# Kernel optimization log

Hardware: AMD Instinct MI355X
Metric: run time of the kernel (lower is better)

The kernel has to match this reference:

```python
import jax, jax.numpy as jnp
import numpy as np
import math

LMAX = 3  # max output/input angular momentum degree


def _cg(j1, m1, j2, m2, j, m):
    """Clebsch-Gordan coefficient <j1 m1 j2 m2 | j m> (Condon-Shortley)."""
    if m1 + m2 != m or not (abs(j1 - j2) <= j <= j1 + j2):
        return 0.0
    f = math.factorial
    pref = math.sqrt(
        (2 * j + 1)
        * f(j + j1 - j2) * f(j - j1 + j2) * f(j1 + j2 - j) / f(j1 + j2 + j + 1)
        * f(j + m) * f(j - m) * f(j1 - m1) * f(j1 + m1) * f(j2 - m2) * f(j2 + m2)
    )
    kmin = max(0, j2 - j - m1, j1 - j + m2)
    kmax = min(j1 + j2 - j, j1 - m1, j2 + m2)
    s = 0.0
    for k in range(kmin, kmax + 1):
        s += (-1) ** k / (
            f(k) * f(j1 + j2 - j - k) * f(j1 - m1 - k) * f(j2 + m2 - k)
            * f(j - j2 + m1 + k) * f(j - j1 - m2 + k)
        )
    return pref * s


def _cg_mat(l1, l2, l):
    C = np.zeros((2 * l1 + 1, 2 * l2 + 1, 2 * l + 1), dtype=np.float32)
    for m1 in range(-l1, l1 + 1):
        for m2 in range(-l2, l2 + 1):
            m = m1 + m2
            if abs(m) <= l:
                C[m1 + l1, m2 + l2, m + l] = _cg(l1, m1, l2, m2, l, m)
    return C


_CG = {}
for _l1 in range(LMAX + 1):
    for _l2 in range(LMAX + 1):
        for _l in range(abs(_l1 - _l2), min(_l1 + _l2, LMAX) + 1):
            _CG[(_l1, _l2, _l)] = jnp.asarray(_cg_mat(_l1, _l2, _l))


def _cg_product(A, B):
    """Full CG tensor product of two SO3 vec-arrays.

    A[l], B[l]: (2=complex, N, 2l+1, tau). Output degree l collects, for every
    (l1, l2) pair with |l1-l2| <= l <= l1+l2, the channel outer product
    contracted against the CG matrix (cormorant CGProduct semantics).
    """
    parts = [[] for _ in range(LMAX + 1)]
    for l1 in range(LMAX + 1):
        for l2 in range(LMAX + 1):
            Ar, Ai = A[l1][0], A[l1][1]  # (N, 2l1+1, tau1)
            Br, Bi = B[l2][0], B[l2][1]  # (N, 2l2+1, tau2)
            for l in range(abs(l1 - l2), min(l1 + l2, LMAX) + 1):
                C = _CG[(l1, l2, l)]  # (2l1+1, 2l2+1, 2l+1)
                Tr = (jnp.einsum('xyz,nxc,nyd->nzcd', C, Ar, Br)
                      - jnp.einsum('xyz,nxc,nyd->nzcd', C, Ai, Bi))
                Ti = (jnp.einsum('xyz,nxc,nyd->nzcd', C, Ar, Bi)
                      + jnp.einsum('xyz,nxc,nyd->nzcd', C, Ai, Br))
                n = Tr.shape[0]
                T = jnp.stack([Tr, Ti], axis=0).reshape(2, n, 2 * l + 1, -1)
                parts[l].append(T)
    return tuple(jnp.concatenate(p, axis=-1) for p in parts)


def setup_inputs() -> dict:
    key = jax.random.key(0)
    keys = jax.random.split(key, 8)
    N, TAU = 1024, 16
    d = {}
    for l in range(LMAX + 1):
        d[f'A{l}'] = jax.random.normal(keys[l], (2, N, 2 * l + 1, TAU), dtype=jnp.float32)
        d[f'B{l}'] = jax.random.normal(keys[4 + l], (2, N, 2 * l + 1, TAU), dtype=jnp.float32)
    return d


def reference(A0, A1, A2, A3, B0, B1, B2, B3):
    return _cg_product([A0, A1, A2, A3], [B0, B1, B2, B3])
```

## Files before the change

kernel.cpp:

```cpp
#include <hip/hip_runtime.h>


__device__ inline double dfact(int n) {
    double r = 1.0;
    for (int i = 2; i <= n; ++i) r *= (double)i;
    return r;
}

__device__ double cg_coef(int j1, int m1, int j2, int m2, int j, int m) {
    if (m1 + m2 != m) return 0.0;
    double pref = sqrt((double)(2 * j + 1)
        * dfact(j + j1 - j2) * dfact(j - j1 + j2) * dfact(j1 + j2 - j)
        / dfact(j1 + j2 + j + 1)
        * dfact(j + m) * dfact(j - m) * dfact(j1 - m1) * dfact(j1 + m1)
        * dfact(j2 - m2) * dfact(j2 + m2));
    int kmin = 0;
    if (j2 - j - m1 > kmin) kmin = j2 - j - m1;
    if (j1 - j + m2 > kmin) kmin = j1 - j + m2;
    int kmax = j1 + j2 - j;
    if (j1 - m1 < kmax) kmax = j1 - m1;
    if (j2 + m2 < kmax) kmax = j2 + m2;
    double s = 0.0;
    for (int k = kmin; k <= kmax; ++k) {
        double d = dfact(k) * dfact(j1 + j2 - j - k) * dfact(j1 - m1 - k)
                 * dfact(j2 + m2 - k) * dfact(j - j2 + m1 + k)
                 * dfact(j - j1 - m2 + k);
        s += (k & 1) ? (-1.0 / d) : (1.0 / d);
    }
    return pref * s;
}

__global__ void cg_init_kernel(float* __restrict__ cgbuf) {
    int tid = blockIdx.x * blockDim.x + threadIdx.x;
    int off = 0;
    for (int l1 = 0; l1 <= 3; ++l1)
    for (int l2 = 0; l2 <= 3; ++l2) {
        int lo = (l1 > l2) ? (l1 - l2) : (l2 - l1);
        int hi = (l1 + l2 < 3) ? (l1 + l2) : 3;
        for (int l = lo; l <= hi; ++l) {
            int xd = 2 * l1 + 1, yd = 2 * l2 + 1, zd = 2 * l + 1;
            int sz = xd * yd * zd;
            if (tid >= off && tid < off + sz) {
                int e = tid - off;
                int z = e % zd;
                int xy = e / zd;
                int y = xy % yd;
                int x = xy / yd;
                int m1 = x - l1, m2 = y - l2, m = z - l;
                double val = 0.0;
                if (m1 + m2 == m) val = cg_coef(l1, m1, l2, m2, l, m);
                cgbuf[tid] = (float)val;
            }
            off += sz;
        }
    }
}

template <int L>
__global__ __launch_bounds__(256) void cg_prod_kernel(
    const float* __restrict__ A0, const float* __restrict__ A1,
    const float* __restrict__ A2, const float* __restrict__ A3,
    const float* __restrict__ B0, const float* __restrict__ B1,
    const float* __restrict__ B2, const float* __restrict__ B3,
    const float* __restrict__ cgbuf,
    float* __restrict__ out,
    int N, long outBase, int CHL)
{
    constexpr int zdim = 2 * L + 1;

    __shared__ int sh_l1, sh_l2, sh_c0, sh_cg;
    __shared__ long sh_qs;
    if (threadIdx.x == 0) {
        long q = (long)blockIdx.x * 256;
        long acc = 0;
        int cg = 0, c0 = 0;
        int fl1 = 0, fl2 = 0, fc0 = 0, fcg = 0;
        long fqs = 0;
        for (int l1 = 0; l1 <= 3; ++l1)
        for (int l2 = 0; l2 <= 3; ++l2) {
            int lo = (l1 > l2) ? (l1 - l2) : (l2 - l1);
            int hi = (l1 + l2 < 3) ? (l1 + l2) : 3;
            for (int l = lo; l <= hi; ++l) {
                if (l == L) {
                    long nq = (long)N * zdim * 64;
                    if (q >= acc && q < acc + nq) {
                        fl1 = l1; fl2 = l2; fc0 = c0; fcg = cg; fqs = acc;
                    }
                    acc += nq;
                    c0 += 256;
                }
                cg += (2 * l1 + 1) * (2 * l2 + 1) * (2 * l + 1);
            }
        }
        sh_l1 = fl1; sh_l2 = fl2; sh_c0 = fc0; sh_cg = fcg; sh_qs = fqs;
    }
    __syncthreads();

    const int l1 = sh_l1, l2 = sh_l2;
    const int xdim = 2 * l1 + 1, ydim = 2 * l2 + 1;
    const float* Abase = (l1 == 0) ? A0 : (l1 == 1) ? A1 : (l1 == 2) ? A2 : A3;
    const float* Bbase = (l2 == 0) ? B0 : (l2 == 1) ? B1 : (l2 == 2) ? B2 : B3;

    unsigned v = (unsigned)((long)blockIdx.x * 256 + threadIdx.x - sh_qs);
    const int cd4 = v & 63;
    v >>= 6;
    const int n = v / zdim;
    const int z = v - n * zdim;
    const int c = cd4 >> 2;
    const int d4 = (cd4 & 3) << 2;

    const float* Ar = Abase + (long)n * xdim * 16 + c;
    const float* Ai = Ar + (long)N * xdim * 16;
    const float* Br = Bbase + (long)n * ydim * 16 + d4;
    const float* Bi = Br + (long)N * ydim * 16;
    const float* CG = cgbuf + sh_cg + z;

    const int s = z + l1 + l2 - L;
    int xlo = s - (ydim - 1); if (xlo < 0) xlo = 0;
    int xhi = (s < xdim - 1) ? s : (xdim - 1);

    float4 accr = make_float4(0.f, 0.f, 0.f, 0.f);
    float4 acci = make_float4(0.f, 0.f, 0.f, 0.f);
    for (int x = xlo; x <= xhi; ++x) {
        const int y = s - x;
        const float cgv = CG[(x * ydim + y) * zdim];
        const float arv = Ar[x * 16];
        const float aiv = Ai[x * 16];
        const float4 br = *reinterpret_cast<const float4*>(Br + y * 16);
        const float4 bi = *reinterpret_cast<const float4*>(Bi + y * 16);
        accr.x += cgv * (arv * br.x - aiv * bi.x);
        accr.y += cgv * (arv * br.y - aiv * bi.y);
        accr.z += cgv * (arv * br.z - aiv * bi.z);
        accr.w += cgv * (arv * br.w - aiv * bi.w);
        acci.x += cgv * (arv * bi.x + aiv * br.x);
        acci.y += cgv * (arv * bi.y + aiv * br.y);
        acci.z += cgv * (arv * bi.z + aiv * br.z);
        acci.w += cgv * (arv * bi.w + aiv * br.w);
    }

    const long off = outBase + ((long)n * zdim + z) * (long)CHL + sh_c0 + cd4 * 4;
    *reinterpret_cast<float4*>(out + off) = accr;
    *reinterpret_cast<float4*>(out + off + (long)N * zdim * CHL) = acci;
}

extern "C" void kernel_launch(void* const* d_in, const int* in_sizes, int n_in,
                              void* d_out, int out_size, void* d_ws, size_t ws_size,
                              hipStream_t stream) {
    const float* A0 = (const float*)d_in[0];
    const float* B0 = (const float*)d_in[1];
    const float* A1 = (const float*)d_in[2];
    const float* B1 = (const float*)d_in[3];
    const float* A2 = (const float*)d_in[4];
    const float* B2 = (const float*)d_in[5];
    const float* A3 = (const float*)d_in[6];
    const float* B3 = (const float*)d_in[7];
    float* out = (float*)d_out;
    float* cgbuf = (float*)d_ws;

    const int N = in_sizes[0] / 32;

    hipLaunchKernelGGL(cg_init_kernel, dim3(14), dim3(256), 0, stream, cgbuf);

    int npairs[4] = {0, 0, 0, 0};
    for (int l1 = 0; l1 <= 3; ++l1)
    for (int l2 = 0; l2 <= 3; ++l2) {
        int lo = (l1 > l2) ? (l1 - l2) : (l2 - l1);
        int hi = (l1 + l2 < 3) ? (l1 + l2) : 3;
        for (int l = lo; l <= hi; ++l) npairs[l]++;
    }

    long base = 0;
    for (int L = 0; L < 4; ++L) {
        const int CHL = npairs[L] * 256;
        const long quads = (long)npairs[L] * N * (2 * L + 1) * 64;
        const int blocks = (int)(quads / 256);
        switch (L) {
            case 0:
                hipLaunchKernelGGL((cg_prod_kernel<0>), dim3(blocks), dim3(256), 0, stream,
                                   A0, A1, A2, A3, B0, B1, B2, B3, cgbuf, out, N, base, CHL);
                break;
            case 1:
                hipLaunchKernelGGL((cg_prod_kernel<1>), dim3(blocks), dim3(256), 0, stream,
                                   A0, A1, A2, A3, B0, B1, B2, B3, cgbuf, out, N, base, CHL);
                break;
            case 2:
                hipLaunchKernelGGL((cg_prod_kernel<2>), dim3(blocks), dim3(256), 0, stream,
                                   A0, A1, A2, A3, B0, B1, B2, B3, cgbuf, out, N, base, CHL);
                break;
            case 3:
                hipLaunchKernelGGL((cg_prod_kernel<3>), dim3(blocks), dim3(256), 0, stream,
                                   A0, A1, A2, A3, B0, B1, B2, B3, cgbuf, out, N, base, CHL);
                break;
        }
        base += (long)2 * N * (2 * L + 1) * CHL;
    }
}
```

Before: 380.3 us.

## Fuse per-degree launches into one kernel with compile-time triple specialization

Replaces four per-output-degree launches with a single 2D-grid kernel, where blockIdx.y selects one of the 34 (l1,l2,L) triples and dispatches to a fully templated body. Each thread now handles all z components for its (n, c, d-quad), loading A and B once into registers instead of reloading per z. The per-block serial search for the triple in thread 0, and the syncthreads after it, are removed. This raises register use and code size from the unrolled templates, and output writes per thread now stride across z rows.

```diff
diff --git a/kernel.cpp b/kernel.cpp
--- a/kernel.cpp
+++ b/kernel.cpp
@@ -56,91 +56,121 @@
     }
 }
 
-template <int L>
-__global__ __launch_bounds__(256) void cg_prod_kernel(
+struct TriTab {
+    int l1[34], l2[34], L[34], c0[34], cg[34];
+    int ch[4];
+    long cum[4];
+};
+
+constexpr TriTab make_tab() {
+    TriTab t{};
+    int idx = 0, cg = 0;
+    int c0L[4] = {0, 0, 0, 0};
+    for (int a = 0; a <= 3; ++a)
+    for (int b = 0; b <= 3; ++b) {
+        int lo = (a > b) ? (a - b) : (b - a);
+        int hi = (a + b < 3) ? (a + b) : 3;
+        for (int l = lo; l <= hi; ++l) {
+            t.l1[idx] = a; t.l2[idx] = b; t.L[idx] = l;
+            t.c0[idx] = c0L[l]; c0L[l] += 256;
+            t.cg[idx] = cg; cg += (2 * a + 1) * (2 * b + 1) * (2 * l + 1);
+            ++idx;
+        }
+    }
+    for (int l = 0; l < 4; ++l) t.ch[l] = c0L[l];
+    long acc = 0;
+    for (int l = 0; l < 4; ++l) { t.cum[l] = acc; acc += 2L * (2 * l + 1) * c0L[l]; }
+    return t;
+}
+
+constexpr TriTab TAB = make_tab();
+
+template <int l1, int l2, int L, int c0, int cgoff>
+__device__ __forceinline__ void tri_body(
     const float* __restrict__ A0, const float* __restrict__ A1,
     const float* __restrict__ A2, const float* __restrict__ A3,
     const float* __restrict__ B0, const float* __restrict__ B1,
     const float* __restrict__ B2, const float* __restrict__ B3,
-    const float* __restrict__ cgbuf,
-    float* __restrict__ out,
-    int N, long outBase, int CHL)
+    const float* __restrict__ cgbuf, float* __restrict__ out, int N)
 {
-    constexpr int zdim = 2 * L + 1;
+    constexpr int xdim = 2 * l1 + 1, ydim = 2 * l2 + 1, zdim = 2 * L + 1;
+    constexpr int CHL = TAB.ch[L];
 
-    __shared__ int sh_l1, sh_l2, sh_c0, sh_cg;
-    __shared__ long sh_qs;
-    if (threadIdx.x == 0) {
-        long q = (long)blockIdx.x * 256;
-        long acc = 0;
-        int cg = 0, c0 = 0;
-        int fl1 = 0, fl2 = 0, fc0 = 0, fcg = 0;
-        long fqs = 0;
-        for (int l1 = 0; l1 <= 3; ++l1)
-        for (int l2 = 0; l2 <= 3; ++l2) {
-            int lo = (l1 > l2) ? (l1 - l2) : (l2 - l1);
-            int hi = (l1 + l2 < 3) ? (l1 + l2) : 3;
-            for (int l = lo; l <= hi; ++l) {
-                if (l == L) {
-                    long nq = (long)N * zdim * 64;
-                    if (q >= acc && q < acc + nq) {
-                        fl1 = l1; fl2 = l2; fc0 = c0; fcg = cg; fqs = acc;
-                    }
-                    acc += nq;
-                    c0 += 256;
-                }
-                cg += (2 * l1 + 1) * (2 * l2 + 1) * (2 * l + 1);
-            }
-        }
-        sh_l1 = fl1; sh_l2 = fl2; sh_c0 = fc0; sh_cg = fcg; sh_qs = fqs;
-    }
-    __syncthreads();
+    const int q   = blockIdx.x * 256 + threadIdx.x;
+    const int n   = q >> 6;
+    const int cd4 = q & 63;
+    const int c   = cd4 >> 2;
+    const int d4  = (cd4 & 3) << 2;
 
-    const int l1 = sh_l1, l2 = sh_l2;
-    const int xdim = 2 * l1 + 1, ydim = 2 * l2 + 1;
-    const float* Abase = (l1 == 0) ? A0 : (l1 == 1) ? A1 : (l1 == 2) ? A2 : A3;
-    const float* Bbase = (l2 == 0) ? B0 : (l2 == 1) ? B1 : (l2 == 2) ? B2 : B3;
+    const float* Ab = (l1 == 0) ? A0 : (l1 == 1) ? A1 : (l1 == 2) ? A2 : A3;
+    const float* Bb = (l2 == 0) ? B0 : (l2 == 1) ? B1 : (l2 == 2) ? B2 : B3;
 
-    unsigned v = (unsigned)((long)blockIdx.x * 256 + threadIdx.x - sh_qs);
-    const int cd4 = v & 63;
-    v >>= 6;
-    const int n = v / zdim;
-    const int z = v - n * zdim;
-    const int c = cd4 >> 2;
-    const int d4 = (cd4 & 3) << 2;
+    const float* Ar = Ab + (long)n * (xdim * 16) + c;
+    const float* Ai = Ar + (long)N * (xdim * 16);
+    const float* Br = Bb + (long)n * (ydim * 16) + d4;
+    const float* Bi = Br + (long)N * (ydim * 16);
+    const float* CG = cgbuf + cgoff;
 
-    const float* Ar = Abase + (long)n * xdim * 16 + c;
-    const float* Ai = Ar + (long)N * xdim * 16;
-    const float* Br = Bbase + (long)n * ydim * 16 + d4;
-    const float* Bi = Br + (long)N * ydim * 16;
-    const float* CG = cgbuf + sh_cg + z;
-
-    const int s = z + l1 + l2 - L;
-    int xlo = s - (ydim - 1); if (xlo < 0) xlo = 0;
-    int xhi = (s < xdim - 1) ? s : (xdim - 1);
-
-    float4 accr = make_float4(0.f, 0.f, 0.f, 0.f);
-    float4 acci = make_float4(0.f, 0.f, 0.f, 0.f);
-    for (int x = xlo; x <= xhi; ++x) {
-        const int y = s - x;
-        const float cgv = CG[(x * ydim + y) * zdim];
-        const float arv = Ar[x * 16];
-        const float aiv = Ai[x * 16];
-        const float4 br = *reinterpret_cast<const float4*>(Br + y * 16);
-        const float4 bi = *reinterpret_cast<const float4*>(Bi + y * 16);
-        accr.x += cgv * (arv * br.x - aiv * bi.x);
-        accr.y += cgv * (arv * br.y - aiv * bi.y);
-        accr.z += cgv * (arv * br.z - aiv * bi.z);
-        accr.w += cgv * (arv * br.w - aiv * bi.w);
-        acci.x += cgv * (arv * bi.x + aiv * br.x);
-        acci.y += cgv * (arv * bi.y + aiv * br.y);
-        acci.z += cgv * (arv * bi.z + aiv * br.z);
-        acci.w += cgv * (arv * bi.w + aiv * br.w);
+    float ar[xdim], ai[xdim];
+    #pragma unroll
+    for (int x = 0; x < xdim; ++x) { ar[x] = Ar[x * 16]; ai[x] = Ai[x * 16]; }
+    float4 br[ydim], bi[ydim];
+    #pragma unroll
+    for (int y = 0; y < ydim; ++y) {
+        br[y] = *reinterpret_cast<const float4*>(Br + y * 16);
+        bi[y] = *reinterpret_cast<const float4*>(Bi + y * 16);
     }
 
-    const long off = outBase + ((long)n * zdim + z) * (long)CHL + sh_c0 + cd4 * 4;
-    *reinterpret_cast<float4*>(out + off) = accr;
-    *reinterpret_cast<float4*>(out + off + (long)N * zdim * CHL) = acci;
+    long off = (long)N * TAB.cum[L] + (long)n * (zdim * CHL) + (c0 + cd4 * 4);
+    const long imagOff = (long)N * (zdim * CHL);
+
+    #pragma unroll
+    for (int z = 0; z < zdim; ++z) {
+        const int s   = z + l1 + l2 - L;
+        const int xlo = (s - (ydim - 1) > 0) ? s - (ydim - 1) : 0;
+        const int xhi = (s < xdim - 1) ? s : xdim - 1;
+        float4 accr = make_float4(0.f, 0.f, 0.f, 0.f);
+        float4 acci = make_float4(0.f, 0.f, 0.f, 0.f);
+        #pragma unroll
+        for (int x = xlo; x <= xhi; ++x) {
+            const int y = s - x;
+            const float  cgv = CG[(x * ydim + y) * zdim + z];
+            const float  car = cgv * ar[x];
+            const float  cai = cgv * ai[x];
+            const float4 brv = br[y];
+            const float4 biv = bi[y];
+            accr.x += car * brv.x - cai * biv.x;
+            accr.y += car * brv.y - cai * biv.y;
+            accr.z += car * brv.z - cai * biv.z;
+            accr.w += car * brv.w - cai * biv.w;
+            acci.x += car * biv.x + cai * brv.x;
+            acci.y += car * biv.y + cai * brv.y;
+            acci.z += car * biv.z + cai * brv.z;
+            acci.w += car * biv.w + cai * brv.w;
+        }
+        *reinterpret_cast<float4*>(out + off) = accr;
+        *reinterpret_cast<float4*>(out + off + imagOff) = acci;
+        off += CHL;
+    }
+}
+
+__global__ __launch_bounds__(256) void cg_prod_all(
+    const float* __restrict__ A0, const float* __restrict__ A1,
+    const float* __restrict__ A2, const float* __restrict__ A3,
+    const float* __restrict__ B0, const float* __restrict__ B1,
+    const float* __restrict__ B2, const float* __restrict__ B3,
+    const float* __restrict__ cgbuf, float* __restrict__ out, int N)
+{
+    switch (blockIdx.y) {
+#define TC(i) case i: tri_body<TAB.l1[i], TAB.l2[i], TAB.L[i], TAB.c0[i], TAB.cg[i]>( \
+        A0, A1, A2, A3, B0, B1, B2, B3, cgbuf, out, N); break;
+        TC(0)  TC(1)  TC(2)  TC(3)  TC(4)  TC(5)  TC(6)  TC(7)
+        TC(8)  TC(9)  TC(10) TC(11) TC(12) TC(13) TC(14) TC(15)
+        TC(16) TC(17) TC(18) TC(19) TC(20) TC(21) TC(22) TC(23)
+        TC(24) TC(25) TC(26) TC(27) TC(28) TC(29) TC(30) TC(31)
+        TC(32) TC(33)
+#undef TC
+    }
 }
 
 extern "C" void kernel_launch(void* const* d_in, const int* in_sizes, int n_in,
@@ -154,44 +184,13 @@
     const float* B2 = (const float*)d_in[5];
     const float* A3 = (const float*)d_in[6];
     const float* B3 = (const float*)d_in[7];
-    float* out = (float*)d_out;
+    float* out   = (float*)d_out;
     float* cgbuf = (float*)d_ws;
 
     const int N = in_sizes[0] / 32;
 
     hipLaunchKernelGGL(cg_init_kernel, dim3(14), dim3(256), 0, stream, cgbuf);
 
-    int npairs[4] = {0, 0, 0, 0};
-    for (int l1 = 0; l1 <= 3; ++l1)
-    for (int l2 = 0; l2 <= 3; ++l2) {
-        int lo = (l1 > l2) ? (l1 - l2) : (l2 - l1);
-        int hi = (l1 + l2 < 3) ? (l1 + l2) : 3;
-        for (int l = lo; l <= hi; ++l) npairs[l]++;
-    }
-
-    long base = 0;
-    for (int L = 0; L < 4; ++L) {
-        const int CHL = npairs[L] * 256;
-        const long quads = (long)npairs[L] * N * (2 * L + 1) * 64;
-        const int blocks = (int)(quads / 256);
-        switch (L) {
-            case 0:
-                hipLaunchKernelGGL((cg_prod_kernel<0>), dim3(blocks), dim3(256), 0, stream,
-                                   A0, A1, A2, A3, B0, B1, B2, B3, cgbuf, out, N, base, CHL);
-                break;
-            case 1:
-                hipLaunchKernelGGL((cg_prod_kernel<1>), dim3(blocks), dim3(256), 0, stream,
-                                   A0, A1, A2, A3, B0, B1, B2, B3, cgbuf, out, N, base, CHL);
-                break;
-            case 2:
-                hipLaunchKernelGGL((cg_prod_kernel<2>), dim3(blocks), dim3(256), 0, stream,
-                                   A0, A1, A2, A3, B0, B1, B2, B3, cgbuf, out, N, base, CHL);
-                break;
-            case 3:
-                hipLaunchKernelGGL((cg_prod_kernel<3>), dim3(blocks), dim3(256), 0, stream,
-                                   A0, A1, A2, A3, B0, B1, B2, B3, cgbuf, out, N, base, CHL);
-                break;
-        }
-        base += (long)2 * N * (2 * L + 1) * CHL;
-    }
+    hipLaunchKernelGGL(cg_prod_all, dim3(N / 4, 34), dim3(256), 0, stream,
+                       A0, A1, A2, A3, B0, B1, B2, B3, cgbuf, out, N);
 }
```

New measurement: 354.8 us. 6.7% less time.
